# Performance work log

Hardware: AMD Instinct MI355X
Metric: run time of the kernel (lower is better)

## Reference

```python
import jax, jax.numpy as jnp
import numpy as np

H = 8            # num_heads
WIN = 128        # num_windows (sliding-window half-width)
B, T, C = 2, 4096, 512


def setup_inputs() -> dict:
    key = jax.random.key(0)
    k1, k2, k3 = jax.random.split(key, 3)
    x = jax.random.normal(k1, (B, T, C), dtype=jnp.float32)
    W_qkv = jax.random.normal(k2, (C, 3 * C), dtype=jnp.float32) * (C ** -0.5)
    W_out = jax.random.normal(k3, (C, C), dtype=jnp.float32) * (C ** -0.5)
    b_out = jnp.zeros((C,), dtype=jnp.float32)
    return {"x": x, "W_qkv": W_qkv, "W_out": W_out, "b_out": b_out}


def reference(x, W_qkv, W_out, b_out):
    Bx, Tx, Cx = x.shape
    hd = Cx // H
    scale = hd ** -0.5
    # qkv projection -> [B, T, 3, H, hd]
    qkv = (x @ W_qkv).reshape(Bx, Tx, 3, H, hd)
    q, k, v = qkv[:, :, 0], qkv[:, :, 1], qkv[:, :, 2]  # each [B, T, H, hd]
    # attention scores [B, H, T, T]
    scores = jnp.einsum('bihd,bjhd->bhij', q, k) * scale
    idx = jnp.arange(Tx)
    band = jnp.abs(idx[:, None] - idx[None, :]) <= WIN  # [T, T] bool
    scores = jnp.where(band[None, None], scores, jnp.float32(-jnp.inf))
    attn = jax.nn.softmax(scores, axis=-1)
    # dropout is identity in eval mode (p handled by config; omitted)
    out = jnp.einsum('bhij,bjhd->bihd', attn, v).reshape(Bx, Tx, Cx)
    return out @ W_out + b_out
```

## Files before the change

### kernel.cpp

```cpp
#include <hip/hip_runtime.h>
#include <stdint.h>

typedef unsigned short ushort_t;
typedef __attribute__((ext_vector_type(8))) __bf16 bf16x8;
typedef __attribute__((ext_vector_type(8))) unsigned short ushortx8;
typedef __attribute__((ext_vector_type(4))) float floatx4;
typedef __attribute__((ext_vector_type(4))) unsigned int uint4v;

__device__ inline ushort_t f2bf(float f) {
  union { float f; unsigned u; } v; v.f = f;
  unsigned r = v.u + 0x7FFFu + ((v.u >> 16) & 1u);
  return (ushort_t)(r >> 16);
}

__device__ inline floatx4 mfma16(bf16x8 a, bf16x8 b, floatx4 c) {
  return __builtin_amdgcn_mfma_f32_16x16x32_bf16(a, b, c, 0, 0, 0);
}

__device__ inline void gload_lds16(const ushort_t* g, ushort_t* l) {
  __builtin_amdgcn_global_load_lds((__attribute__((address_space(1))) void*)(void*)(g),
                                   (__attribute__((address_space(3))) void*)(l),
                                   16, 0, 0);
}

__global__ __launch_bounds__(256) void k_conv_x(const float* __restrict__ x,
                                                ushort_t* __restrict__ xb) {
  int i = (blockIdx.x * 256 + threadIdx.x) * 4;
  float4 v = *(const float4*)(x + i);
  ushort4 o;
  o.x = f2bf(v.x); o.y = f2bf(v.y); o.z = f2bf(v.z); o.w = f2bf(v.w);
  *(ushort4*)(xb + i) = o;
}

__global__ __launch_bounds__(256) void k_conv_wT(const float* __restrict__ src,
                                                 ushort_t* __restrict__ dst, int N) {
  __shared__ float tile[32][33];
  int tid = threadIdx.x;
  int k0 = blockIdx.x * 32, n0 = blockIdx.y * 32;
  int c = tid & 31, r0 = tid >> 5;
#pragma unroll
  for (int i = 0; i < 4; ++i) {
    int r = r0 + i * 8;
    tile[r][c] = src[(size_t)(k0 + r) * N + n0 + c];
  }
  __syncthreads();
#pragma unroll
  for (int i = 0; i < 4; ++i) {
    int r = r0 + i * 8;
    dst[(size_t)(n0 + r) * 512 + k0 + c] = f2bf(tile[c][r]);
  }
}

template <int EPI>
__global__ __launch_bounds__(256)
void k_gemm_bt(const ushort_t* __restrict__ A, const ushort_t* __restrict__ Bt,
               ushort_t* __restrict__ qd, ushort_t* __restrict__ kd, ushort_t* __restrict__ vd,
               float* __restrict__ outf, const float* __restrict__ bias) {
  __shared__ __align__(16) ushort_t As[8 * 512];
  __shared__ __align__(16) ushort_t Bs[8 * 512];
  const int tid = threadIdx.x;
  const int w = tid >> 6, l = tid & 63;
  const int lr = l & 15, lq = l >> 4;
  const int m0 = blockIdx.x * 128, n0 = blockIdx.y * 128;
  const int wm = w >> 1, wn = w & 1;

  floatx4 acc[4][4];
#pragma unroll
  for (int i = 0; i < 4; ++i)
#pragma unroll
    for (int j = 0; j < 4; ++j) acc[i][j] = (floatx4)0.0f;

  for (int k0 = 0; k0 < 512; k0 += 32) {
#pragma unroll
    for (int c2 = 0; c2 < 2; ++c2) {
      int blk = w * 2 + c2;
      gload_lds16(A + (size_t)(m0 + blk * 16 + lr) * 512 + k0 + lq * 8, &As[blk * 512]);
      gload_lds16(Bt + (size_t)(n0 + blk * 16 + lr) * 512 + k0 + lq * 8, &Bs[blk * 512]);
    }
    __syncthreads();
    bf16x8 af[4], bfr[4];
#pragma unroll
    for (int i = 0; i < 4; ++i) af[i] = *(const bf16x8*)&As[(wm * 4 + i) * 512 + l * 8];
#pragma unroll
    for (int i = 0; i < 4; ++i) bfr[i] = *(const bf16x8*)&Bs[(wn * 4 + i) * 512 + l * 8];
#pragma unroll
    for (int i = 0; i < 4; ++i)
#pragma unroll
      for (int j = 0; j < 4; ++j) acc[i][j] = mfma16(af[i], bfr[j], acc[i][j]);
    __syncthreads();
  }

#pragma unroll
  for (int i = 0; i < 4; ++i) {
#pragma unroll
    for (int j = 0; j < 4; ++j) {
      int n = n0 + wn * 64 + j * 16 + lr;
      if (EPI == 0) {
        int which = n >> 9, h = (n >> 6) & 7, d = n & 63;
        ushort_t* dst = (which == 0) ? qd : (which == 1) ? kd : vd;
#pragma unroll
        for (int r = 0; r < 4; ++r) {
          int m = m0 + wm * 64 + i * 16 + lq * 4 + r;
          int b = m >> 12, t = m & 4095;
          dst[(((size_t)(b * 8 + h)) * 4096 + t) * 64 + d] = f2bf(acc[i][j][r]);
        }
      } else {
        float bv = bias[n];
#pragma unroll
        for (int r = 0; r < 4; ++r) {
          int m = m0 + wm * 64 + i * 16 + lq * 4 + r;
          outf[(size_t)m * 512 + n] = acc[i][j][r] + bv;
        }
      }
    }
  }
}

__global__ __launch_bounds__(256) void k_transpose_v(const ushort_t* __restrict__ v,
                                                     ushort_t* __restrict__ vt) {
  __shared__ __align__(16) ushort_t lt[64][72];
  int tid = threadIdx.x, w = tid >> 6, l = tid & 63;
  int bh = blockIdx.y, t0 = blockIdx.x * 64;
  int row = w * 16 + (l & 15), ch = (l >> 4) * 16;
  const ushort_t* src = v + ((size_t)bh * 4096 + t0 + row) * 64 + ch;
  *(ushortx8*)&lt[row][ch] = *(const ushortx8*)src;
  *(ushortx8*)&lt[row][ch + 8] = *(const ushortx8*)(src + 8);
  __syncthreads();
  ushortx8 o0, o1;
#pragma unroll
  for (int i = 0; i < 8; ++i) o0[i] = lt[w * 16 + i][l];
#pragma unroll
  for (int i = 0; i < 8; ++i) o1[i] = lt[w * 16 + 8 + i][l];
  ushort_t* dst = vt + ((size_t)bh * 64 + l) * 4096 + t0 + w * 16;
  *(ushortx8*)dst = o0;
  *(ushortx8*)(dst + 8) = o1;
}

__global__ __launch_bounds__(256)
void k_attn(const ushort_t* __restrict__ qa, const ushort_t* __restrict__ ka,
            const ushort_t* __restrict__ vta, ushort_t* __restrict__ ao) {
  __shared__ __align__(16) ushort_t Vs[40 * 512];
  const int tid = threadIdx.x, w = tid >> 6, l = tid & 63;
  const int lr = l & 15, lq = l >> 4;
  const int bh = blockIdx.y, qt0 = blockIdx.x * 64;
  const int qrow = qt0 + w * 16;

  const ushort_t* vbase = vta + (size_t)bh * 64 * 4096;
#pragma unroll
  for (int i = 0; i < 10; ++i) {
    int t = w * 10 + i;
    int kt2 = t >> 2, nt = t & 3;
    int d = nt * 16 + lr;
    int key = qt0 - 128 + kt2 * 32 + lq * 8;
    key = min(max(key, 0), 4088);
    gload_lds16(vbase + (size_t)d * 4096 + key, &Vs[t * 512]);
  }

  const ushort_t* qp = qa + ((size_t)bh * 4096 + qrow + lr) * 64 + lq * 8;
  bf16x8 qf0 = *(const bf16x8*)qp;
  bf16x8 qf1 = *(const bf16x8*)(qp + 32);

  const float C = 0.125f * 1.4426950408889634f;
  uint2 pk[18];
  pk[17].x = 0u; pk[17].y = 0u;
  float ps = 0.f;
#pragma unroll
  for (int kt = 0; kt < 17; ++kt) {
    int kb = qrow - 128 + kt * 16;
    int kc = min(max(kb + lr, 0), 4095);
    const ushort_t* kp = ka + ((size_t)bh * 4096 + kc) * 64 + lq * 8;
    bf16x8 kf0 = *(const bf16x8*)kp;
    bf16x8 kf1 = *(const bf16x8*)(kp + 32);
    floatx4 s = (floatx4)0.0f;
    s = mfma16(kf0, qf0, s);
    s = mfma16(kf1, qf1, s);
    float p[4];
#pragma unroll
    for (int r = 0; r < 4; ++r) {
      int r_rel = kt * 16 + lq * 4 + r;
      int kj = qrow - 128 + r_rel;
      bool ok = (kj >= 0) && (kj < 4096) && (r_rel >= lr) && (r_rel - lr <= 256);
      float e = ok ? exp2f(s[r] * C) : 0.f;
      ps += e;
      p[r] = e;
    }
    pk[kt].x = (unsigned)f2bf(p[0]) | ((unsigned)f2bf(p[1]) << 16);
    pk[kt].y = (unsigned)f2bf(p[2]) | ((unsigned)f2bf(p[3]) << 16);
  }

  ps += __shfl_xor(ps, 16, 64);
  ps += __shfl_xor(ps, 32, 64);
  float inv = __builtin_amdgcn_rcpf(ps);

  __syncthreads();

  floatx4 oacc[4];
#pragma unroll
  for (int nt = 0; nt < 4; ++nt) oacc[nt] = (floatx4)0.0f;
  const int srcA = ((l >> 4) & 1) * 32 + lr;
  const int srcB = srcA + 16;
  const bool selhi = (l & 32) != 0;

#pragma unroll
  for (int kk = 0; kk < 9; ++kk) {
    unsigned e0 = __shfl(pk[2 * kk].x, srcA, 64);
    unsigned e1 = __shfl(pk[2 * kk].y, srcA, 64);
    unsigned e2 = __shfl(pk[2 * kk].x, srcB, 64);
    unsigned e3 = __shfl(pk[2 * kk].y, srcB, 64);
    unsigned o0 = __shfl(pk[2 * kk + 1].x, srcA, 64);
    unsigned o1 = __shfl(pk[2 * kk + 1].y, srcA, 64);
    unsigned o2 = __shfl(pk[2 * kk + 1].x, srcB, 64);
    unsigned o3 = __shfl(pk[2 * kk + 1].y, srcB, 64);
    union { uint4v u; bf16x8 b; } pu;
    pu.u[0] = selhi ? o0 : e0;
    pu.u[1] = selhi ? o1 : e1;
    pu.u[2] = selhi ? o2 : e2;
    pu.u[3] = selhi ? o3 : e3;

    int keyrel = w * 16 + kk * 32 + lq * 8;
    keyrel = min(keyrel, 312);
    int kt2 = keyrel >> 5, seg = (keyrel >> 3) & 3;
    const ushort_t* vsp = &Vs[kt2 * 2048 + seg * 128 + lr * 8];
#pragma unroll
    for (int nt = 0; nt < 4; ++nt) {
      bf16x8 vf = *(const bf16x8*)(vsp + nt * 512);
      oacc[nt] = mfma16(pu.b, vf, oacc[nt]);
    }
  }

  float invr[4];
#pragma unroll
  for (int r = 0; r < 4; ++r) invr[r] = __shfl(inv, lq * 4 + r, 64);

  int b = bh >> 3, h = bh & 7;
#pragma unroll
  for (int nt = 0; nt < 4; ++nt)
#pragma unroll
    for (int r = 0; r < 4; ++r) {
      int t = qrow + lq * 4 + r;
      int col = h * 64 + nt * 16 + lr;
      ao[((size_t)(b * 4096 + t)) * 512 + col] = f2bf(oacc[nt][r] * invr[r]);
    }
}

extern "C" void kernel_launch(void* const* d_in, const int* in_sizes, int n_in,
                              void* d_out, int out_size, void* d_ws, size_t ws_size,
                              hipStream_t stream) {
  const float* x    = (const float*)d_in[0];
  const float* Wqkv = (const float*)d_in[1];
  const float* Wout = (const float*)d_in[2];
  const float* bout = (const float*)d_in[3];
  float* out = (float*)d_out;
  char* ws = (char*)d_ws;
  const size_t MB = 1024 * 1024;

  ushort_t* xb    = (ushort_t*)(ws);
  ushort_t* wqkvT = (ushort_t*)(ws + 8 * MB);
  ushort_t* woutT = (ushort_t*)(ws + 9 * MB + MB/2);
  ushort_t* q     = (ushort_t*)(ws + 10 * MB);
  ushort_t* k     = (ushort_t*)(ws + 18 * MB);
  ushort_t* v     = (ushort_t*)(ws + 26 * MB);
  ushort_t* vt    = (ushort_t*)(ws + 34 * MB);
  ushort_t* ao    = xb;

  k_conv_x<<<4096, 256, 0, stream>>>(x, xb);
  k_conv_wT<<<dim3(16, 48), 256, 0, stream>>>(Wqkv, wqkvT, 1536);
  k_conv_wT<<<dim3(16, 16), 256, 0, stream>>>(Wout, woutT, 512);
  k_gemm_bt<0><<<dim3(64, 12), 256, 0, stream>>>(xb, wqkvT, q, k, v, nullptr, nullptr);
  k_transpose_v<<<dim3(64, 16), 256, 0, stream>>>(v, vt);
  k_attn<<<dim3(64, 16), 256, 0, stream>>>(q, k, vt, ao);
  k_gemm_bt<1><<<dim3(64, 4), 256, 0, stream>>>(ao, woutT, nullptr, nullptr, nullptr, out, bout);
}
```

Baseline: 158.9 us.

## Fuse prep conversions into one launch, double GEMM K-step, shrink output GEMM tile

Merges the x conversion and both weight transposes into a single kernel launch, which removes two launch gaps. The GEMM now stages a K-slice of 64 per sync instead of 32, halving the number of barriers. It is templated on the M tile size, and the output projection uses 64-row tiles so it launches 512 blocks instead of 256, filling more CUs. LDS use per block grows, which may lower occupancy for the QKV GEMM.

```diff
diff --git a/kernel.cpp b/kernel.cpp
--- a/kernel.cpp
+++ b/kernel.cpp
@@ -23,20 +23,24 @@
                                    16, 0, 0);
 }
 
-__global__ __launch_bounds__(256) void k_conv_x(const float* __restrict__ x,
-                                                ushort_t* __restrict__ xb) {
-  int i = (blockIdx.x * 256 + threadIdx.x) * 4;
-  float4 v = *(const float4*)(x + i);
-  ushort4 o;
-  o.x = f2bf(v.x); o.y = f2bf(v.y); o.z = f2bf(v.z); o.w = f2bf(v.w);
-  *(ushort4*)(xb + i) = o;
-}
-
-__global__ __launch_bounds__(256) void k_conv_wT(const float* __restrict__ src,
-                                                 ushort_t* __restrict__ dst, int N) {
+__global__ __launch_bounds__(256)
+void k_prep(const float* __restrict__ x, ushort_t* __restrict__ xb,
+            const float* __restrict__ Wqkv, ushort_t* __restrict__ wqkvT,
+            const float* __restrict__ Wout, ushort_t* __restrict__ woutT) {
+  int bx = blockIdx.x, tid = threadIdx.x;
+  if (bx < 4096) {
+    int i = (bx * 256 + tid) * 4;
+    float4 v = *(const float4*)(x + i);
+    ushort4 o;
+    o.x = f2bf(v.x); o.y = f2bf(v.y); o.z = f2bf(v.z); o.w = f2bf(v.w);
+    *(ushort4*)(xb + i) = o;
+    return;
+  }
   __shared__ float tile[32][33];
-  int tid = threadIdx.x;
-  int k0 = blockIdx.x * 32, n0 = blockIdx.y * 32;
+  const float* src; ushort_t* dst; int N, id;
+  if (bx < 4096 + 768) { id = bx - 4096; src = Wqkv; dst = wqkvT; N = 1536; }
+  else                 { id = bx - 4864; src = Wout; dst = woutT; N = 512;  }
+  int k0 = (id & 15) * 32, n0 = (id >> 4) * 32;
   int c = tid & 31, r0 = tid >> 5;
 #pragma unroll
   for (int i = 0; i < 4; ++i) {
@@ -51,47 +55,64 @@
   }
 }
 
-template <int EPI>
+template <int EPI, int MT>
 __global__ __launch_bounds__(256)
 void k_gemm_bt(const ushort_t* __restrict__ A, const ushort_t* __restrict__ Bt,
                ushort_t* __restrict__ qd, ushort_t* __restrict__ kd, ushort_t* __restrict__ vd,
                float* __restrict__ outf, const float* __restrict__ bias) {
-  __shared__ __align__(16) ushort_t As[8 * 512];
-  __shared__ __align__(16) ushort_t Bs[8 * 512];
+  constexpr int ABLK = MT / 16;
+  constexpr int AISS = ABLK * 2;
+  constexpr int TOT  = AISS + 16;
+  constexpr int PER  = TOT / 4;
+  constexpr int IT   = MT / 32;
+  __shared__ __align__(16) ushort_t As[ABLK * 1024];
+  __shared__ __align__(16) ushort_t Bs[8 * 1024];
   const int tid = threadIdx.x;
   const int w = tid >> 6, l = tid & 63;
   const int lr = l & 15, lq = l >> 4;
-  const int m0 = blockIdx.x * 128, n0 = blockIdx.y * 128;
+  const int m0 = blockIdx.x * MT, n0 = blockIdx.y * 128;
   const int wm = w >> 1, wn = w & 1;
 
-  floatx4 acc[4][4];
-#pragma unroll
-  for (int i = 0; i < 4; ++i)
+  floatx4 acc[IT][4];
+#pragma unroll
+  for (int i = 0; i < IT; ++i)
 #pragma unroll
     for (int j = 0; j < 4; ++j) acc[i][j] = (floatx4)0.0f;
 
-  for (int k0 = 0; k0 < 512; k0 += 32) {
-#pragma unroll
-    for (int c2 = 0; c2 < 2; ++c2) {
-      int blk = w * 2 + c2;
-      gload_lds16(A + (size_t)(m0 + blk * 16 + lr) * 512 + k0 + lq * 8, &As[blk * 512]);
-      gload_lds16(Bt + (size_t)(n0 + blk * 16 + lr) * 512 + k0 + lq * 8, &Bs[blk * 512]);
+  for (int k0 = 0; k0 < 512; k0 += 64) {
+#pragma unroll
+    for (int i = 0; i < PER; ++i) {
+      int idx = w * PER + i;
+      if (idx < AISS) {
+        int blk = idx >> 1, half = idx & 1;
+        gload_lds16(A + (size_t)(m0 + blk * 16 + lr) * 512 + k0 + half * 32 + lq * 8,
+                    &As[blk * 1024 + half * 512]);
+      } else {
+        int j = idx - AISS, blk = j >> 1, half = j & 1;
+        gload_lds16(Bt + (size_t)(n0 + blk * 16 + lr) * 512 + k0 + half * 32 + lq * 8,
+                    &Bs[blk * 1024 + half * 512]);
+      }
     }
     __syncthreads();
-    bf16x8 af[4], bfr[4];
-#pragma unroll
-    for (int i = 0; i < 4; ++i) af[i] = *(const bf16x8*)&As[(wm * 4 + i) * 512 + l * 8];
-#pragma unroll
-    for (int i = 0; i < 4; ++i) bfr[i] = *(const bf16x8*)&Bs[(wn * 4 + i) * 512 + l * 8];
-#pragma unroll
-    for (int i = 0; i < 4; ++i)
-#pragma unroll
-      for (int j = 0; j < 4; ++j) acc[i][j] = mfma16(af[i], bfr[j], acc[i][j]);
+#pragma unroll
+    for (int half = 0; half < 2; ++half) {
+      bf16x8 af[IT], bfr[4];
+#pragma unroll
+      for (int i = 0; i < IT; ++i)
+        af[i] = *(const bf16x8*)&As[(wm * IT + i) * 1024 + half * 512 + l * 8];
+#pragma unroll
+      for (int j = 0; j < 4; ++j)
+        bfr[j] = *(const bf16x8*)&Bs[(wn * 4 + j) * 1024 + half * 512 + l * 8];
+#pragma unroll
+      for (int i = 0; i < IT; ++i)
+#pragma unroll
+        for (int j = 0; j < 4; ++j) acc[i][j] = mfma16(af[i], bfr[j], acc[i][j]);
+    }
     __syncthreads();
   }
 
 #pragma unroll
-  for (int i = 0; i < 4; ++i) {
+  for (int i = 0; i < IT; ++i) {
 #pragma unroll
     for (int j = 0; j < 4; ++j) {
       int n = n0 + wn * 64 + j * 16 + lr;
@@ -100,7 +121,7 @@
         ushort_t* dst = (which == 0) ? qd : (which == 1) ? kd : vd;
 #pragma unroll
         for (int r = 0; r < 4; ++r) {
-          int m = m0 + wm * 64 + i * 16 + lq * 4 + r;
+          int m = m0 + wm * (IT * 16) + i * 16 + lq * 4 + r;
           int b = m >> 12, t = m & 4095;
           dst[(((size_t)(b * 8 + h)) * 4096 + t) * 64 + d] = f2bf(acc[i][j][r]);
         }
@@ -108,7 +129,7 @@
         float bv = bias[n];
 #pragma unroll
         for (int r = 0; r < 4; ++r) {
-          int m = m0 + wm * 64 + i * 16 + lq * 4 + r;
+          int m = m0 + wm * (IT * 16) + i * 16 + lq * 4 + r;
           outf[(size_t)m * 512 + n] = acc[i][j][r] + bv;
         }
       }
@@ -263,11 +284,9 @@
   ushort_t* vt    = (ushort_t*)(ws + 34 * MB);
   ushort_t* ao    = xb;
 
-  k_conv_x<<<4096, 256, 0, stream>>>(x, xb);
-  k_conv_wT<<<dim3(16, 48), 256, 0, stream>>>(Wqkv, wqkvT, 1536);
-  k_conv_wT<<<dim3(16, 16), 256, 0, stream>>>(Wout, woutT, 512);
-  k_gemm_bt<0><<<dim3(64, 12), 256, 0, stream>>>(xb, wqkvT, q, k, v, nullptr, nullptr);
+  k_prep<<<5120, 256, 0, stream>>>(x, xb, Wqkv, wqkvT, Wout, woutT);
+  k_gemm_bt<0, 128><<<dim3(64, 12), 256, 0, stream>>>(xb, wqkvT, q, k, v, nullptr, nullptr);
   k_transpose_v<<<dim3(64, 16), 256, 0, stream>>>(v, vt);
   k_attn<<<dim3(64, 16), 256, 0, stream>>>(q, k, vt, ao);
-  k_gemm_bt<1><<<dim3(64, 4), 256, 0, stream>>>(ao, woutT, nullptr, nullptr, nullptr, out, bout);
-}
+  k_gemm_bt<1, 64><<<dim3(128, 4), 256, 0, stream>>>(ao, woutT, nullptr, nullptr, nullptr, out, bout);
+}
```

Measured after the change: 156.7 us. About the same (-1.4%).
